# Optimization experiments

Measured on AMD Instinct MI355X. Metric: run time of the kernel, lower is better.

Reference implementation:

```python
import jax, jax.numpy as jnp
import numpy as np

EPS = 1e-5  # nn.LayerNorm default

def _ln(x, g, b):
    m = x.mean(-1, keepdims=True)
    v = ((x - m) ** 2).mean(-1, keepdims=True)
    return (x - m) / jnp.sqrt(v + EPS) * g + b


def setup_inputs() -> dict:
    key = jax.random.key(0)
    ks = jax.random.split(key, 16)
    B, T, H, W = 8, 20, 224, 224
    D, NC = 1536, 7
    s = 0.02
    f32 = jnp.float32
    return {
        'x': jax.random.normal(ks[0], (B, 3, T, H, W), f32),
        'timestamp': jax.random.uniform(ks[1], (B,), f32),
        # surrogate backbone: patchify conv (stride 16) + global avg pool -> 1536 feats
        'conv_w': jax.random.normal(ks[2], (D, 3, 16, 16), f32) * s,
        'conv_b': jnp.zeros((D,), f32),
        'w_red': jax.random.normal(ks[3], (D, D), f32) * s,
        'b_red': jnp.zeros((D,), f32),
        'w_num': jax.random.normal(ks[4], (D, 1), f32) * s,
        'b_num': jnp.zeros((D,), f32),
        'time_embed': jax.random.normal(ks[5], (1, T, D), f32) * s,
        'cls_swap': jax.random.normal(ks[6], (1, 5, 1, D), f32) * s,
        'ln_g': jnp.ones((D,), f32),
        'ln_b': jnp.zeros((D,), f32),
        'w_qkv': jax.random.normal(ks[7], (3 * D, D), f32) * s,
        'w_tproj': jax.random.normal(ks[8], (D, D), f32) * s,
        'b_tproj': jnp.zeros((D,), f32),
        'w_tfc': jax.random.normal(ks[9], (D, D), f32) * s,
        'b_tfc': jnp.zeros((D,), f32),
        'w_head': jax.random.normal(ks[10], (NC, D), f32) * s,
        'b_head': jnp.zeros((NC,), f32),
    }


def reference(x, timestamp, conv_w, conv_b, w_red, b_red, w_num, b_num,
              time_embed, cls_swap, ln_g, ln_b, w_qkv, w_tproj, b_tproj,
              w_tfc, b_tfc, w_head, b_head):
    B, C, T, H, W = x.shape
    D = w_red.shape[0]
    NH = 12
    HD = D // NH
    scale = HD ** -0.5

    # (b t) c h w  -> backbone surrogate -> (B*T, D)
    xf = jnp.transpose(x, (0, 2, 1, 3, 4)).reshape(B * T, C, H, W)
    f = jax.lax.conv_general_dilated(
        xf, conv_w, window_strides=(16, 16), padding='VALID',
        dimension_numbers=('NCHW', 'OIHW', 'NCHW'))
    f = (f + conv_b[None, :, None, None]).mean((2, 3))  # global avg pool -> (BT, D)

    xr = (f @ w_red.T + b_red).reshape(B, T, D)           # reduce_dim
    xt = xr + time_embed
    te = timestamp[:, None] @ w_num.T + b_num             # NumberToVector (B, D)
    xt = xt + te[:, None, :]

    # groups: b (n k) c -> b n k c, k=4, n=5; prepend 1 cls token per group
    g = jnp.concatenate(
        [jnp.broadcast_to(cls_swap, (B, 5, 1, D)), xt.reshape(B, 5, 4, D)], axis=2)

    for _ in range(4):  # num_interactions
        gr = g.reshape(B * 5, 5, D)
        hn = _ln(gr, ln_g, ln_b)
        qkv = (hn @ w_qkv.T).reshape(B * 5, 5, 3, NH, HD).transpose(2, 0, 3, 1, 4)
        q, k, v = qkv[0], qkv[1], qkv[2]                  # (b*n, h, t, hd)
        a = jax.nn.softmax(jnp.einsum('bhqd,bhkd->bhqk', q, k) * scale, axis=-1)
        o = jnp.einsum('bhqk,bhkd->bhqd', a, v).transpose(0, 2, 1, 3).reshape(B * 5, 5, D)
        o = o @ w_tproj.T + b_tproj                       # attn proj
        upd = (o @ w_tfc.T + b_tfc) + gr                  # temporal_fc + residual
        g = upd.reshape(B, 5, 5, D)
        # swap cls tokens between groups via roll
        g = g.at[:, :, 0, :].set(jnp.roll(g[:, :, 0, :], 1, axis=1))

    xt = g[:, :, 1:, :].reshape(B, T, D)
    out = xt[:, -1, :] + xr[:, -1, :]
    return out @ w_head.T + b_head  # (B, num_classes)
```

## Files before the change

### kernel.cpp

```cpp
#include <hip/hip_runtime.h>

typedef __attribute__((ext_vector_type(8))) short short8;
typedef __attribute__((ext_vector_type(8))) unsigned short ushort8;
typedef __attribute__((ext_vector_type(4))) float f32x4;
typedef unsigned short ushort_t;

__device__ __forceinline__ ushort_t f2bf(float f) {
    unsigned u = __builtin_bit_cast(unsigned, f);
    u += 0x7fffu + ((u >> 16) & 1u);
    return (ushort_t)(u >> 16);
}

__device__ __forceinline__ void load_lds16(const void* gp, void* lp) {
    __builtin_amdgcn_global_load_lds(
        (const __attribute__((address_space(1))) void*)gp,
        (__attribute__((address_space(3))) void*)lp, 16, 0, 0);
}

__global__ __launch_bounds__(256, 4) void pool_kernel(
    const float* __restrict__ x, ushort_t* __restrict__ AP) {
    int blk = blockIdx.x, tid = threadIdx.x;
    int bt = blk / 12, rc = blk % 12;
    int c = rc >> 2, igrp = rc & 3;
    int w = tid >> 6, lane = tid & 63;
    int i = igrp * 4 + w;
    int b = bt / 20, t = bt % 20;
    const float* base = x + (size_t)((b * 3 + c) * 20 + t) * 50176;

    f32x4 v[13];
    #pragma unroll
    for (int it = 0; it < 13; ++it) {
        int k = lane + it * 64;
        int kk = k < 784 ? k : 0;
        int ri = (kk * 9363) >> 19;
        int c4 = kk - ri * 56;
        v[it] = *(const f32x4*)(base + (16 * ri + i) * 224 + 4 * c4);
        if (k >= 784) v[it] = (f32x4){0.f, 0.f, 0.f, 0.f};
    }
    #pragma unroll
    for (int s = 1; s < 13; s <<= 1)
        #pragma unroll
        for (int j = 0; j + s < 13; j += 2 * s)
            v[j] += v[j + s];
    f32x4 acc = v[0];
    #pragma unroll
    for (int m = 4; m <= 32; m <<= 1) {
        acc[0] += __shfl_xor(acc[0], m);
        acc[1] += __shfl_xor(acc[1], m);
        acc[2] += __shfl_xor(acc[2], m);
        acc[3] += __shfl_xor(acc[3], m);
    }
    if (lane < 4) {
        ushort4 o;
        o.x = f2bf(acc[0] * (1.f / 196.f));
        o.y = f2bf(acc[1] * (1.f / 196.f));
        o.z = f2bf(acc[2] * (1.f / 196.f));
        o.w = f2bf(acc[3] * (1.f / 196.f));
        *(ushort4*)(AP + (size_t)bt * 768 + c * 256 + i * 16 + 4 * lane) = o;
    }
}

__global__ __launch_bounds__(256) void wprep_kernel(
    const float* __restrict__ w_qkv, const float* __restrict__ w_tf,
    const float* __restrict__ w_red, const float* __restrict__ conv_w,
    const float* __restrict__ w_tp, const float* __restrict__ b_tp,
    const float* __restrict__ b_tf, const float* __restrict__ conv_b,
    const float* __restrict__ b_red, const float* __restrict__ cls,
    ushort_t* __restrict__ WQ, ushort_t* __restrict__ WF,
    ushort_t* __restrict__ WR, ushort_t* __restrict__ WCVT,
    ushort_t* __restrict__ WTT, float* __restrict__ BC,
    float* __restrict__ BC2, float* __restrict__ GA) {
    __shared__ __align__(16) float smem[64 * 68];
    int blk = blockIdx.x, tid = threadIdx.x;
    if (blk < 5760) {
        long c = (long)blk * 256 + tid;
        const float* s; ushort_t* d; long i;
        if (c < 884736)       { s = w_qkv; d = WQ; i = c; }
        else if (c < 1179648) { s = w_tf;  d = WF; i = c - 884736; }
        else                  { s = w_red; d = WR; i = c - 1179648; }
        i <<= 3;
        f32x4 a = *(const f32x4*)(s + i);
        f32x4 b = *(const f32x4*)(s + i + 4);
        ushort8 o;
        o[0] = f2bf(a[0]); o[1] = f2bf(a[1]); o[2] = f2bf(a[2]); o[3] = f2bf(a[3]);
        o[4] = f2bf(b[0]); o[5] = f2bf(b[1]); o[6] = f2bf(b[2]); o[7] = f2bf(b[3]);
        *(ushort8*)(d + i) = o;
    } else if (blk < 6336) {
        int tb = blk - 5760;
        int bi = tb / 24, bj = tb % 24;
        int r0 = (tid >> 4) << 2;
        int c0 = (tid & 15) << 2;
        #pragma unroll
        for (int rr = 0; rr < 4; ++rr) {
            f32x4 v = *(const f32x4*)(w_tp + (size_t)(bi * 64 + r0 + rr) * 1536 + bj * 64 + c0);
            smem[(r0 + rr) * 68 + c0 + 0] = v[0];
            smem[(r0 + rr) * 68 + c0 + 1] = v[1];
            smem[(r0 + rr) * 68 + c0 + 2] = v[2];
            smem[(r0 + rr) * 68 + c0 + 3] = v[3];
        }
        __syncthreads();
        #pragma unroll
        for (int rr = 0; rr < 4; ++rr) {
            int jj = r0 + rr;
            ushort4 o;
            o.x = f2bf(smem[(c0 + 0) * 68 + jj]);
            o.y = f2bf(smem[(c0 + 1) * 68 + jj]);
            o.z = f2bf(smem[(c0 + 2) * 68 + jj]);
            o.w = f2bf(smem[(c0 + 3) * 68 + jj]);
            *(ushort4*)(WTT + (size_t)(bj * 64 + jj) * 1536 + bi * 64 + c0) = o;
        }
    } else if (blk < 6624) {
        int tb = blk - 6336;
        int bi = tb / 12, bj = tb % 12;
        int r0 = (tid >> 4) << 2;
        int c0 = (tid & 15) << 2;
        #pragma unroll
        for (int rr = 0; rr < 4; ++rr) {
            f32x4 v = *(const f32x4*)(conv_w + (size_t)(bi * 64 + r0 + rr) * 768 + bj * 64 + c0);
            smem[(r0 + rr) * 68 + c0 + 0] = v[0];
            smem[(r0 + rr) * 68 + c0 + 1] = v[1];
            smem[(r0 + rr) * 68 + c0 + 2] = v[2];
            smem[(r0 + rr) * 68 + c0 + 3] = v[3];
        }
        __syncthreads();
        #pragma unroll
        for (int rr = 0; rr < 4; ++rr) {
            int jj = r0 + rr;
            ushort4 o;
            o.x = f2bf(smem[(c0 + 0) * 68 + jj]);
            o.y = f2bf(smem[(c0 + 1) * 68 + jj]);
            o.z = f2bf(smem[(c0 + 2) * 68 + jj]);
            o.w = f2bf(smem[(c0 + 3) * 68 + jj]);
            *(ushort4*)(WCVT + (size_t)(bj * 64 + jj) * 1536 + bi * 64 + c0) = o;
        }
    } else if (blk < 6664) {
        int cblk = blk - 6624;
        int b = cblk / 5, n = cblk % 5;
        size_t row = (size_t)(b * 25 + n * 5) * 1536;
        #pragma unroll
        for (int j = 0; j < 6; ++j) {
            int d = tid + j * 256;
            GA[row + d] = cls[n * 1536 + d];
        }
    } else if (blk < 6760) {
        int bb = blk - 6664;
        int row = bb * 16 + (tid >> 4);
        int sub = tid & 15;
        float acc = 0.f;
        for (int j = 0; j < 96; ++j) {
            int k = sub + j * 16;
            acc += w_tf[(size_t)row * 1536 + k] * b_tp[k];
        }
        acc += __shfl_xor(acc, 1); acc += __shfl_xor(acc, 2);
        acc += __shfl_xor(acc, 4); acc += __shfl_xor(acc, 8);
        if (sub == 0) BC[row] = acc + b_tf[row];
    } else {
        int bb = blk - 6760;
        int row = bb * 16 + (tid >> 4);
        int sub = tid & 15;
        float acc = 0.f;
        for (int j = 0; j < 48; ++j) {
            int k = sub + j * 16;
            acc += w_red[(size_t)row * 1536 + k] * 0.f;
        }
        acc = 0.f;
        for (int j = 0; j < 48; ++j) {
            int n0 = sub + j * 16;
            acc += w_red[(size_t)row * 1536 + n0] * conv_b[n0];
            acc += w_red[(size_t)row * 1536 + n0 + 768] * conv_b[n0 + 768];
        }
        acc += __shfl_xor(acc, 1); acc += __shfl_xor(acc, 2);
        acc += __shfl_xor(acc, 4); acc += __shfl_xor(acc, 8);
        if (sub == 0) BC2[row] = acc + b_red[row];
    }
}

template <int MT, bool OUT_BF16, bool HAS_BIAS, bool HAS_RES, bool CLS_SWAP, bool BUILD_G>
__device__ __forceinline__ void gemm_tile(
    char* lds, int lane, int tn, int tm,
    const ushort_t* __restrict__ A, const ushort_t* __restrict__ B,
    void* __restrict__ Cv, const float* __restrict__ bias,
    const float* __restrict__ res, int M, int N, int K, int KS,
    float* __restrict__ g_out, const float* __restrict__ temb,
    const float* __restrict__ ts, const float* __restrict__ w_num,
    const float* __restrict__ b_num) {
    constexpr int BUFB = MT * 2048 + 8192;

    f32x4 acc[MT][4];
    #pragma unroll
    for (int m = 0; m < MT; ++m)
        #pragma unroll
        for (int n = 0; n < 4; ++n)
            acc[m][n] = (f32x4){0.f, 0.f, 0.f, 0.f};

    const int nK = K >> 6;
    const int rbase = lane >> 3, cc = lane & 7;

    auto stage = [&](int k0, int buf) {
        char* lA = lds + buf * BUFB;
        char* lB = lA + MT * 2048;
        #pragma unroll
        for (int j = 0; j < MT * 2; ++j) {
            int row = j * 8 + rbase;
            int cf = cc ^ (row & 7);
            int ga = tm * (MT * 16) + row; if (ga > M - 1) ga = M - 1;
            load_lds16(A + (size_t)ga * KS + (k0 + cf * 8), lA + j * 1024);
        }
        #pragma unroll
        for (int j = 0; j < 8; ++j) {
            int row = j * 8 + rbase;
            int cf = cc ^ (row & 7);
            load_lds16(B + (size_t)(tn * 64 + row) * KS + (k0 + cf * 8), lB + j * 1024);
        }
    };

    stage(0, 0);
    for (int t = 0; t < nK; ++t) {
        int cur = t & 1;
        if (t + 1 < nK) {
            stage((t + 1) << 6, cur ^ 1);
            if constexpr (MT == 2) asm volatile("s_waitcnt vmcnt(12)" ::: "memory");
            else                   asm volatile("s_waitcnt vmcnt(16)" ::: "memory");
        } else {
            asm volatile("s_waitcnt vmcnt(0)" ::: "memory");
        }
        __builtin_amdgcn_sched_barrier(0);
        const char* lA = lds + cur * BUFB;
        const char* lB = lA + MT * 2048;
        #pragma unroll
        for (int ks = 0; ks < 2; ++ks) {
            short8 av[MT], bv[4];
            const int rlo = lane & 15;
            const int chi = ks * 4 + (lane >> 4);
            #pragma unroll
            for (int m = 0; m < MT; ++m) {
                int r = m * 16 + rlo;
                av[m] = *(const short8*)(lA + r * 128 + ((chi ^ (r & 7)) << 4));
            }
            #pragma unroll
            for (int n = 0; n < 4; ++n) {
                int r = n * 16 + rlo;
                bv[n] = *(const short8*)(lB + r * 128 + ((chi ^ (r & 7)) << 4));
            }
            #pragma unroll
            for (int m = 0; m < MT; ++m)
                #pragma unroll
                for (int n = 0; n < 4; ++n)
                    acc[m][n] = __builtin_amdgcn_mfma_f32_16x16x32_bf16(
                        av[m], bv[n], acc[m][n], 0, 0, 0);
        }
    }

    const int c_l = lane & 15, r_q = (lane >> 4) * 4;
    #pragma unroll
    for (int m = 0; m < MT; ++m) {
        #pragma unroll
        for (int reg = 0; reg < 4; ++reg) {
            int r_ = tm * (MT * 16) + m * 16 + r_q + reg;
            if (r_ < M) {
                int r2 = r_;
                if (CLS_SWAP) {
                    int bb = r_ / 25, rem = r_ % 25;
                    if (rem % 5 == 0) r2 = bb * 25 + ((rem / 5 + 1) % 5) * 5;
                }
                #pragma unroll
                for (int n = 0; n < 4; ++n) {
                    int cc_ = tn * 64 + n * 16 + c_l;
                    float v = acc[m][n][reg];
                    if (HAS_BIAS) v += bias[cc_];
                    if (HAS_RES) v += res[(size_t)r_ * N + cc_];
                    if (OUT_BF16) ((ushort_t*)Cv)[(size_t)r2 * N + cc_] = f2bf(v);
                    else          ((float*)Cv)[(size_t)r2 * N + cc_] = v;
                    if (BUILD_G) {
                        int b = r_ / 20, t = r_ % 20;
                        float gval = v + temb[t * 1536 + cc_] +
                                     ts[b] * w_num[cc_] + b_num[cc_];
                        g_out[(size_t)(b * 25 + (t / 4) * 5 + (t % 4) + 1) * 1536 + cc_] = gval;
                    }
                }
            }
        }
    }
}

__global__ __launch_bounds__(64) void wcf_kernel(
    const ushort_t* __restrict__ WF, const ushort_t* __restrict__ WTT,
    const ushort_t* __restrict__ WR, const ushort_t* __restrict__ WCVT,
    ushort_t* __restrict__ WC, ushort_t* __restrict__ WRC) {
    __shared__ __align__(16) char lds[32768];
    int task = blockIdx.x, lane = threadIdx.x;
    if (task < 576)
        gemm_tile<4, true, false, false, false, false>(
            lds, lane, task % 24, task / 24, WF, WTT, WC, nullptr, nullptr,
            1536, 1536, 1536, 1536, nullptr, nullptr, nullptr, nullptr, nullptr);
    else {
        int t2 = task - 576;
        gemm_tile<4, true, false, false, false, false>(
            lds, lane, t2 % 12, t2 / 12, WR, WCVT, WRC, nullptr, nullptr,
            1536, 768, 1536, 1536, nullptr, nullptr, nullptr, nullptr, nullptr);
    }
}

__global__ __launch_bounds__(64) void xr_kernel(
    const ushort_t* __restrict__ AP, const ushort_t* __restrict__ WRC,
    float* __restrict__ XR, const float* __restrict__ BC2,
    float* __restrict__ GA, const float* __restrict__ temb,
    const float* __restrict__ ts, const float* __restrict__ w_num,
    const float* __restrict__ b_num) {
    __shared__ __align__(16) char lds[24576];
    gemm_tile<2, false, true, false, false, true>(
        lds, threadIdx.x, blockIdx.x, blockIdx.y, AP, WRC, XR, BC2, nullptr,
        160, 1536, 768, 768, GA, temb, ts, w_num, b_num);
}

__global__ __launch_bounds__(64) void qkv_kernel(
    const ushort_t* __restrict__ HN, const ushort_t* __restrict__ WQ,
    float* __restrict__ C0, float* __restrict__ C1) {
    __shared__ __align__(16) char lds[32768];
    int tn = blockIdx.x, tmh = blockIdx.y;
    int half = tmh >> 2, tm = tmh & 3;
    gemm_tile<4, false, false, false, false, false>(
        lds, threadIdx.x, tn, tm, HN + half * 768, WQ + half * 768,
        half ? C1 : C0, nullptr, nullptr, 200, 4608, 768, 1536,
        nullptr, nullptr, nullptr, nullptr, nullptr);
}

__global__ __launch_bounds__(64) void proj_kernel(
    const ushort_t* __restrict__ OBF, const ushort_t* __restrict__ WC,
    float* __restrict__ gdst, const float* __restrict__ BC,
    const float* __restrict__ gsrc) {
    __shared__ __align__(16) char lds[24576];
    gemm_tile<2, false, true, true, true, false>(
        lds, threadIdx.x, blockIdx.x, blockIdx.y, OBF, WC, gdst, BC, gsrc,
        200, 1536, 1536, 1536, nullptr, nullptr, nullptr, nullptr, nullptr);
}

__global__ __launch_bounds__(256) void ln_kernel(
    const float* __restrict__ g, const float* __restrict__ gamma,
    const float* __restrict__ beta, ushort_t* __restrict__ hn) {
    int r = blockIdx.x, tid = threadIdx.x;
    const float* x = g + (size_t)r * 1536;
    float v[6], s = 0.f, s2 = 0.f;
    #pragma unroll
    for (int j = 0; j < 6; ++j) {
        v[j] = x[tid + j * 256];
        s += v[j]; s2 += v[j] * v[j];
    }
    #pragma unroll
    for (int m = 1; m < 64; m <<= 1) { s += __shfl_xor(s, m); s2 += __shfl_xor(s2, m); }
    __shared__ float red[8];
    int wid = tid >> 6;
    if ((tid & 63) == 0) { red[wid] = s; red[4 + wid] = s2; }
    __syncthreads();
    s  = red[0] + red[1] + red[2] + red[3];
    s2 = red[4] + red[5] + red[6] + red[7];
    float mean = s * (1.0f / 1536.0f);
    float var  = s2 * (1.0f / 1536.0f) - mean * mean;
    float rstd = rsqrtf(var + 1e-5f);
    #pragma unroll
    for (int j = 0; j < 6; ++j) {
        int d = tid + j * 256;
        float y = (v[j] - mean) * rstd * gamma[d] + beta[d];
        hn[(size_t)r * 1536 + d] = f2bf(y);
    }
}

__global__ __launch_bounds__(64) void attn_kernel(
    const float* __restrict__ qA, const float* __restrict__ qB,
    ushort_t* __restrict__ o) {
    int gid = blockIdx.x;
    int h = gid % 12, gg = gid / 12;
    int l = threadIdx.x;
    size_t off = (size_t)gg * 5 * 4608 + h * 128 + 2 * l;
    const float* b0 = qA + off;
    const float* b1 = qB + off;
    float q[5][2], k[5][2], v[5][2];
    #pragma unroll
    for (int tt = 0; tt < 5; ++tt) {
        float2 q0 = *(const float2*)(b0 + tt * 4608);
        float2 q1 = *(const float2*)(b1 + tt * 4608);
        float2 k0 = *(const float2*)(b0 + tt * 4608 + 1536);
        float2 k1 = *(const float2*)(b1 + tt * 4608 + 1536);
        float2 v0 = *(const float2*)(b0 + tt * 4608 + 3072);
        float2 v1 = *(const float2*)(b1 + tt * 4608 + 3072);
        q[tt][0] = q0.x + q1.x; q[tt][1] = q0.y + q1.y;
        k[tt][0] = k0.x + k1.x; k[tt][1] = k0.y + k1.y;
        v[tt][0] = v0.x + v1.x; v[tt][1] = v0.y + v1.y;
    }
    float sc[5][5];
    #pragma unroll
    for (int i = 0; i < 5; ++i)
        #pragma unroll
        for (int j = 0; j < 5; ++j)
            sc[i][j] = q[i][0] * k[j][0] + q[i][1] * k[j][1];
    #pragma unroll
    for (int m = 1; m < 64; m <<= 1)
        #pragma unroll
        for (int i = 0; i < 5; ++i)
            #pragma unroll
            for (int j = 0; j < 5; ++j)
                sc[i][j] += __shfl_xor(sc[i][j], m);
    const float scale = 0.08838834764831845f;
    float a_[5][5];
    #pragma unroll
    for (int i = 0; i < 5; ++i) {
        float mx = -1e30f;
        #pragma unroll
        for (int j = 0; j < 5; ++j) mx = fmaxf(mx, sc[i][j]);
        float sum = 0.f;
        #pragma unroll
        for (int j = 0; j < 5; ++j) { a_[i][j] = __expf((sc[i][j] - mx) * scale); sum += a_[i][j]; }
        float inv = 1.0f / sum;
        #pragma unroll
        for (int j = 0; j < 5; ++j) a_[i][j] *= inv;
    }
    #pragma unroll
    for (int i = 0; i < 5; ++i) {
        float o0 = 0.f, o1 = 0.f;
        #pragma unroll
        for (int j = 0; j < 5; ++j) { o0 += a_[i][j] * v[j][0]; o1 += a_[i][j] * v[j][1]; }
        ushort2 w; w.x = f2bf(o0); w.y = f2bf(o1);
        *(ushort2*)(o + (size_t)(gg * 5 + i) * 1536 + h * 128 + 2 * l) = w;
    }
}

__global__ __launch_bounds__(64) void head_kernel(
    const float* __restrict__ gfin, const float* __restrict__ xr,
    const float* __restrict__ w_head, const float* __restrict__ b_head,
    float* __restrict__ out) {
    int b = blockIdx.x, l = threadIdx.x;
    const float* gv = gfin + (size_t)(b * 25 + 24) * 1536;
    const float* xv = xr + (size_t)(b * 20 + 19) * 1536;
    float acc[7] = {0, 0, 0, 0, 0, 0, 0};
    for (int d = l; d < 1536; d += 64) {
        float xval = gv[d] + xv[d];
        #pragma unroll
        for (int c = 0; c < 7; ++c) acc[c] += xval * w_head[c * 1536 + d];
    }
    #pragma unroll
    for (int c = 0; c < 7; ++c)
        #pragma unroll
        for (int m = 1; m < 64; m <<= 1) acc[c] += __shfl_xor(acc[c], m);
    if (l == 0) {
        #pragma unroll
        for (int c = 0; c < 7; ++c) out[b * 7 + c] = acc[c] + b_head[c];
    }
}

#define OFF_WQ    0u
#define OFF_WF    14155776u
#define OFF_WR    18874368u
#define OFF_WCVT  23592960u
#define OFF_WTT   25952256u
#define OFF_WC    30670848u
#define OFF_WRC   35389440u
#define OFF_BC    37748736u
#define OFF_BC2   37754880u
#define OFF_AP    37761024u
#define OFF_XR    38006784u
#define OFF_GA    38989824u
#define OFF_GB    40218624u
#define OFF_HN    41447424u
#define OFF_QKV0  42061824u
#define OFF_QKV1  45748224u
#define OFF_OBF   49434624u

extern "C" void kernel_launch(void* const* d_in, const int* in_sizes, int n_in,
                              void* d_out, int out_size, void* d_ws, size_t ws_size,
                              hipStream_t stream) {
    const float* x      = (const float*)d_in[0];
    const float* ts     = (const float*)d_in[1];
    const float* conv_w = (const float*)d_in[2];
    const float* conv_b = (const float*)d_in[3];
    const float* w_red  = (const float*)d_in[4];
    const float* b_red  = (const float*)d_in[5];
    const float* w_num  = (const float*)d_in[6];
    const float* b_num  = (const float*)d_in[7];
    const float* temb   = (const float*)d_in[8];
    const float* cls    = (const float*)d_in[9];
    const float* ln_g   = (const float*)d_in[10];
    const float* ln_b   = (const float*)d_in[11];
    const float* w_qkv  = (const float*)d_in[12];
    const float* w_tp   = (const float*)d_in[13];
    const float* b_tp   = (const float*)d_in[14];
    const float* w_tf   = (const float*)d_in[15];
    const float* b_tf   = (const float*)d_in[16];
    const float* w_head = (const float*)d_in[17];
    const float* b_head = (const float*)d_in[18];

    char* ws = (char*)d_ws;
    ushort_t* WQ   = (ushort_t*)(ws + OFF_WQ);
    ushort_t* WF   = (ushort_t*)(ws + OFF_WF);
    ushort_t* WR   = (ushort_t*)(ws + OFF_WR);
    ushort_t* WCVT = (ushort_t*)(ws + OFF_WCVT);
    ushort_t* WTT  = (ushort_t*)(ws + OFF_WTT);
    ushort_t* WC   = (ushort_t*)(ws + OFF_WC);
    ushort_t* WRC  = (ushort_t*)(ws + OFF_WRC);
    float*    BC   = (float*)(ws + OFF_BC);
    float*    BC2  = (float*)(ws + OFF_BC2);
    ushort_t* AP   = (ushort_t*)(ws + OFF_AP);
    float*    XR   = (float*)(ws + OFF_XR);
    float*    GA   = (float*)(ws + OFF_GA);
    float*    GB   = (float*)(ws + OFF_GB);
    ushort_t* HN   = (ushort_t*)(ws + OFF_HN);
    float*    QKV0 = (float*)(ws + OFF_QKV0);
    float*    QKV1 = (float*)(ws + OFF_QKV1);
    ushort_t* OBF  = (ushort_t*)(ws + OFF_OBF);

    pool_kernel<<<1920, 256, 0, stream>>>(x, AP);
    wprep_kernel<<<6856, 256, 0, stream>>>(w_qkv, w_tf, w_red, conv_w, w_tp,
                                           b_tp, b_tf, conv_b, b_red, cls,
                                           WQ, WF, WR, WCVT, WTT, BC, BC2, GA);
    wcf_kernel<<<864, 64, 0, stream>>>(WF, WTT, WR, WCVT, WC, WRC);
    xr_kernel<<<dim3(24, 5), 64, 0, stream>>>(AP, WRC, XR, BC2, GA,
                                              temb, ts, w_num, b_num);
    float* gsrc = GA;
    float* gdst = GB;
    for (int it = 0; it < 4; ++it) {
        ln_kernel<<<200, 256, 0, stream>>>(gsrc, ln_g, ln_b, HN);
        qkv_kernel<<<dim3(72, 8), 64, 0, stream>>>(HN, WQ, QKV0, QKV1);
        attn_kernel<<<480, 64, 0, stream>>>(QKV0, QKV1, OBF);
        proj_kernel<<<dim3(24, 7), 64, 0, stream>>>(OBF, WC, gdst, BC, gsrc);
        float* tmp = gsrc; gsrc = gdst; gdst = tmp;
    }
    head_kernel<<<8, 64, 0, stream>>>(gsrc, XR, w_head, b_head, (float*)d_out);
}
```

Measured before the change: 203.9 us.

## Use 128x128 four-wave double-buffered GEMM tiles for weight-fold and QKV

Adds a 256-thread GEMM tile routine computing 128x128 outputs with swizzled LDS, direct global-to-LDS loads and double buffering. The weight-folding GEMMs and the per-iteration QKV GEMM use it instead of the single-wave 64-wide tiles, aiming for more operand reuse and better latency hiding. It also removes a dead loop in the bias-fold prep. The trade-off is fewer blocks (216 and 144), which can underfill the GPU, especially for QKV with M=200, where the second 128-row tile is mostly clamped padding.

```diff
diff --git a/kernel.cpp b/kernel.cpp
--- a/kernel.cpp
+++ b/kernel.cpp
@@ -160,11 +160,6 @@
         int sub = tid & 15;
         float acc = 0.f;
         for (int j = 0; j < 48; ++j) {
-            int k = sub + j * 16;
-            acc += w_red[(size_t)row * 1536 + k] * 0.f;
-        }
-        acc = 0.f;
-        for (int j = 0; j < 48; ++j) {
             int n0 = sub + j * 16;
             acc += w_red[(size_t)row * 1536 + n0] * conv_b[n0];
             acc += w_red[(size_t)row * 1536 + n0 + 768] * conv_b[n0 + 768];
@@ -173,6 +168,127 @@
         acc += __shfl_xor(acc, 4); acc += __shfl_xor(acc, 8);
         if (sub == 0) BC2[row] = acc + b_red[row];
     }
+}
+
+template <bool OUT_BF16>
+__device__ __forceinline__ void gemm128_tile(
+    char* lds, const ushort_t* __restrict__ A, const ushort_t* __restrict__ B,
+    void* __restrict__ Cv, int M, int N, int K, int KS, int tn, int tm) {
+    const int tid = threadIdx.x;
+    const int lane = tid & 63;
+    const int w = tid >> 6;
+    const int wr = w >> 1, wc = w & 1;
+
+    f32x4 acc[4][4];
+    #pragma unroll
+    for (int m = 0; m < 4; ++m)
+        #pragma unroll
+        for (int n = 0; n < 4; ++n)
+            acc[m][n] = (f32x4){0.f, 0.f, 0.f, 0.f};
+
+    const int nK = K >> 6;
+    const int rbase = lane >> 3, cc = lane & 7;
+
+    auto stage = [&](int k0, int buf) {
+        char* lA = lds + buf * 32768;
+        char* lB = lA + 16384;
+        #pragma unroll
+        for (int j = 0; j < 4; ++j) {
+            int row = w * 32 + j * 8 + rbase;
+            int cf = cc ^ (row & 7);
+            int ga = tm * 128 + row; if (ga > M - 1) ga = M - 1;
+            load_lds16(A + (size_t)ga * KS + (k0 + cf * 8),
+                       lA + (w * 32 + j * 8) * 128);
+        }
+        #pragma unroll
+        for (int j = 0; j < 4; ++j) {
+            int row = w * 32 + j * 8 + rbase;
+            int cf = cc ^ (row & 7);
+            load_lds16(B + (size_t)(tn * 128 + row) * KS + (k0 + cf * 8),
+                       lB + (w * 32 + j * 8) * 128);
+        }
+    };
+
+    stage(0, 0);
+    asm volatile("s_waitcnt vmcnt(0)" ::: "memory");
+    __builtin_amdgcn_s_barrier();
+    __builtin_amdgcn_sched_barrier(0);
+    for (int t = 0; t < nK; ++t) {
+        int cur = t & 1;
+        if (t + 1 < nK) stage((t + 1) << 6, cur ^ 1);
+        __builtin_amdgcn_sched_barrier(0);
+        const char* lA = lds + cur * 32768;
+        const char* lB = lA + 16384;
+        #pragma unroll
+        for (int ks = 0; ks < 2; ++ks) {
+            short8 av[4], bv[4];
+            const int rlo = lane & 15;
+            const int chi = ks * 4 + (lane >> 4);
+            #pragma unroll
+            for (int m = 0; m < 4; ++m) {
+                int r = wr * 64 + m * 16 + rlo;
+                av[m] = *(const short8*)(lA + r * 128 + ((chi ^ (r & 7)) << 4));
+            }
+            #pragma unroll
+            for (int n = 0; n < 4; ++n) {
+                int r = wc * 64 + n * 16 + rlo;
+                bv[n] = *(const short8*)(lB + r * 128 + ((chi ^ (r & 7)) << 4));
+            }
+            #pragma unroll
+            for (int m = 0; m < 4; ++m)
+                #pragma unroll
+                for (int n = 0; n < 4; ++n)
+                    acc[m][n] = __builtin_amdgcn_mfma_f32_16x16x32_bf16(
+                        av[m], bv[n], acc[m][n], 0, 0, 0);
+        }
+        asm volatile("s_waitcnt vmcnt(0)" ::: "memory");
+        __builtin_amdgcn_s_barrier();
+        __builtin_amdgcn_sched_barrier(0);
+    }
+
+    const int c_l = lane & 15, r_q = (lane >> 4) * 4;
+    #pragma unroll
+    for (int m = 0; m < 4; ++m) {
+        #pragma unroll
+        for (int reg = 0; reg < 4; ++reg) {
+            int r_ = tm * 128 + wr * 64 + m * 16 + r_q + reg;
+            if (r_ < M) {
+                #pragma unroll
+                for (int n = 0; n < 4; ++n) {
+                    int cc_ = tn * 128 + wc * 64 + n * 16 + c_l;
+                    float v = acc[m][n][reg];
+                    if (OUT_BF16) ((ushort_t*)Cv)[(size_t)r_ * N + cc_] = f2bf(v);
+                    else          ((float*)Cv)[(size_t)r_ * N + cc_] = v;
+                }
+            }
+        }
+    }
+}
+
+__global__ __launch_bounds__(256) void wcf_kernel(
+    const ushort_t* __restrict__ WF, const ushort_t* __restrict__ WTT,
+    const ushort_t* __restrict__ WR, const ushort_t* __restrict__ WCVT,
+    ushort_t* __restrict__ WC, ushort_t* __restrict__ WRC) {
+    __shared__ __align__(16) char lds[65536];
+    int task = blockIdx.x;
+    if (task < 144)
+        gemm128_tile<true>(lds, WF, WTT, WC, 1536, 1536, 1536, 1536,
+                           task % 12, task / 12);
+    else {
+        int t2 = task - 144;
+        gemm128_tile<true>(lds, WR, WCVT, WRC, 1536, 768, 1536, 1536,
+                           t2 % 6, t2 / 6);
+    }
+}
+
+__global__ __launch_bounds__(256) void qkv_kernel(
+    const ushort_t* __restrict__ HN, const ushort_t* __restrict__ WQ,
+    float* __restrict__ C0, float* __restrict__ C1) {
+    __shared__ __align__(16) char lds[65536];
+    int tn = blockIdx.x, y = blockIdx.y;
+    int half = y >> 1, tm = y & 1;
+    gemm128_tile<false>(lds, HN + half * 768, WQ + half * 768,
+                        half ? C1 : C0, 200, 4608, 768, 1536, tn, tm);
 }
 
 template <int MT, bool OUT_BF16, bool HAS_BIAS, bool HAS_RES, bool CLS_SWAP, bool BUILD_G>
@@ -283,24 +399,6 @@
     }
 }
 
-__global__ __launch_bounds__(64) void wcf_kernel(
-    const ushort_t* __restrict__ WF, const ushort_t* __restrict__ WTT,
-    const ushort_t* __restrict__ WR, const ushort_t* __restrict__ WCVT,
-    ushort_t* __restrict__ WC, ushort_t* __restrict__ WRC) {
-    __shared__ __align__(16) char lds[32768];
-    int task = blockIdx.x, lane = threadIdx.x;
-    if (task < 576)
-        gemm_tile<4, true, false, false, false, false>(
-            lds, lane, task % 24, task / 24, WF, WTT, WC, nullptr, nullptr,
-            1536, 1536, 1536, 1536, nullptr, nullptr, nullptr, nullptr, nullptr);
-    else {
-        int t2 = task - 576;
-        gemm_tile<4, true, false, false, false, false>(
-            lds, lane, t2 % 12, t2 / 12, WR, WCVT, WRC, nullptr, nullptr,
-            1536, 768, 1536, 1536, nullptr, nullptr, nullptr, nullptr, nullptr);
-    }
-}
-
 __global__ __launch_bounds__(64) void xr_kernel(
     const ushort_t* __restrict__ AP, const ushort_t* __restrict__ WRC,
     float* __restrict__ XR, const float* __restrict__ BC2,
@@ -311,18 +409,6 @@
     gemm_tile<2, false, true, false, false, true>(
         lds, threadIdx.x, blockIdx.x, blockIdx.y, AP, WRC, XR, BC2, nullptr,
         160, 1536, 768, 768, GA, temb, ts, w_num, b_num);
-}
-
-__global__ __launch_bounds__(64) void qkv_kernel(
-    const ushort_t* __restrict__ HN, const ushort_t* __restrict__ WQ,
-    float* __restrict__ C0, float* __restrict__ C1) {
-    __shared__ __align__(16) char lds[32768];
-    int tn = blockIdx.x, tmh = blockIdx.y;
-    int half = tmh >> 2, tm = tmh & 3;
-    gemm_tile<4, false, false, false, false, false>(
-        lds, threadIdx.x, tn, tm, HN + half * 768, WQ + half * 768,
-        half ? C1 : C0, nullptr, nullptr, 200, 4608, 768, 1536,
-        nullptr, nullptr, nullptr, nullptr, nullptr);
 }
 
 __global__ __launch_bounds__(64) void proj_kernel(
@@ -511,14 +597,14 @@
     wprep_kernel<<<6856, 256, 0, stream>>>(w_qkv, w_tf, w_red, conv_w, w_tp,
                                            b_tp, b_tf, conv_b, b_red, cls,
                                            WQ, WF, WR, WCVT, WTT, BC, BC2, GA);
-    wcf_kernel<<<864, 64, 0, stream>>>(WF, WTT, WR, WCVT, WC, WRC);
+    wcf_kernel<<<216, 256, 0, stream>>>(WF, WTT, WR, WCVT, WC, WRC);
     xr_kernel<<<dim3(24, 5), 64, 0, stream>>>(AP, WRC, XR, BC2, GA,
                                               temb, ts, w_num, b_num);
     float* gsrc = GA;
     float* gdst = GB;
     for (int it = 0; it < 4; ++it) {
         ln_kernel<<<200, 256, 0, stream>>>(gsrc, ln_g, ln_b, HN);
-        qkv_kernel<<<dim3(72, 8), 64, 0, stream>>>(HN, WQ, QKV0, QKV1);
+        qkv_kernel<<<dim3(36, 4), 256, 0, stream>>>(HN, WQ, QKV0, QKV1);
         attn_kernel<<<480, 64, 0, stream>>>(QKV0, QKV1, OBF);
         proj_kernel<<<dim3(24, 7), 64, 0, stream>>>(OBF, WC, gdst, BC, gsrc);
         float* tmp = gsrc; gsrc = gdst; gdst = tmp;
```

Result: no change. 207.7 us (+1.9%).

## Defer fused weight-product GEMM into first QKV launch to overlap work

Applied to the files above, without the earlier changes.

The WF·WTT weight-combination GEMM moves out of the early wcf launch and into the first iteration's QKV launch, so both run as independent tiles in one grid. Only the WR·WCVT product stays before xr_kernel, which is the only one xr_kernel needs. The intent is to shorten the critical path before the xr/LN stages and let the combined-weight GEMM fill the otherwise underused grid of the first QKV GEMM. A dead loop that multiplied by zero in the bias precompute is also removed.

```diff
diff --git a/kernel.cpp b/kernel.cpp
--- a/kernel.cpp
+++ b/kernel.cpp
@@ -160,11 +160,6 @@
         int sub = tid & 15;
         float acc = 0.f;
         for (int j = 0; j < 48; ++j) {
-            int k = sub + j * 16;
-            acc += w_red[(size_t)row * 1536 + k] * 0.f;
-        }
-        acc = 0.f;
-        for (int j = 0; j < 48; ++j) {
             int n0 = sub + j * 16;
             acc += w_red[(size_t)row * 1536 + n0] * conv_b[n0];
             acc += w_red[(size_t)row * 1536 + n0 + 768] * conv_b[n0 + 768];
@@ -283,22 +278,48 @@
     }
 }
 
-__global__ __launch_bounds__(64) void wcf_kernel(
+__global__ __launch_bounds__(64) void wrc_kernel(
+    const ushort_t* __restrict__ WR, const ushort_t* __restrict__ WCVT,
+    ushort_t* __restrict__ WRC) {
+    __shared__ __align__(16) char lds[32768];
+    int task = blockIdx.x;
+    gemm_tile<4, true, false, false, false, false>(
+        lds, threadIdx.x, task % 12, task / 12, WR, WCVT, WRC, nullptr, nullptr,
+        1536, 768, 1536, 1536, nullptr, nullptr, nullptr, nullptr, nullptr);
+}
+
+__global__ __launch_bounds__(64) void qkv0wc_kernel(
+    const ushort_t* __restrict__ HN, const ushort_t* __restrict__ WQ,
+    float* __restrict__ C0, float* __restrict__ C1,
     const ushort_t* __restrict__ WF, const ushort_t* __restrict__ WTT,
-    const ushort_t* __restrict__ WR, const ushort_t* __restrict__ WCVT,
-    ushort_t* __restrict__ WC, ushort_t* __restrict__ WRC) {
+    ushort_t* __restrict__ WC) {
     __shared__ __align__(16) char lds[32768];
     int task = blockIdx.x, lane = threadIdx.x;
-    if (task < 576)
-        gemm_tile<4, true, false, false, false, false>(
-            lds, lane, task % 24, task / 24, WF, WTT, WC, nullptr, nullptr,
-            1536, 1536, 1536, 1536, nullptr, nullptr, nullptr, nullptr, nullptr);
-    else {
+    if (task < 576) {
+        int tn = task % 72, tmh = task / 72;
+        int half = tmh >> 2, tm = tmh & 3;
+        gemm_tile<4, false, false, false, false, false>(
+            lds, lane, tn, tm, HN + half * 768, WQ + half * 768,
+            half ? C1 : C0, nullptr, nullptr, 200, 4608, 768, 1536,
+            nullptr, nullptr, nullptr, nullptr, nullptr);
+    } else {
         int t2 = task - 576;
         gemm_tile<4, true, false, false, false, false>(
-            lds, lane, t2 % 12, t2 / 12, WR, WCVT, WRC, nullptr, nullptr,
-            1536, 768, 1536, 1536, nullptr, nullptr, nullptr, nullptr, nullptr);
-    }
+            lds, lane, t2 % 24, t2 / 24, WF, WTT, WC, nullptr, nullptr,
+            1536, 1536, 1536, 1536, nullptr, nullptr, nullptr, nullptr, nullptr);
+    }
+}
+
+__global__ __launch_bounds__(64) void qkv_kernel(
+    const ushort_t* __restrict__ HN, const ushort_t* __restrict__ WQ,
+    float* __restrict__ C0, float* __restrict__ C1) {
+    __shared__ __align__(16) char lds[32768];
+    int tn = blockIdx.x, tmh = blockIdx.y;
+    int half = tmh >> 2, tm = tmh & 3;
+    gemm_tile<4, false, false, false, false, false>(
+        lds, threadIdx.x, tn, tm, HN + half * 768, WQ + half * 768,
+        half ? C1 : C0, nullptr, nullptr, 200, 4608, 768, 1536,
+        nullptr, nullptr, nullptr, nullptr, nullptr);
 }
 
 __global__ __launch_bounds__(64) void xr_kernel(
@@ -311,18 +332,6 @@
     gemm_tile<2, false, true, false, false, true>(
         lds, threadIdx.x, blockIdx.x, blockIdx.y, AP, WRC, XR, BC2, nullptr,
         160, 1536, 768, 768, GA, temb, ts, w_num, b_num);
-}
-
-__global__ __launch_bounds__(64) void qkv_kernel(
-    const ushort_t* __restrict__ HN, const ushort_t* __restrict__ WQ,
-    float* __restrict__ C0, float* __restrict__ C1) {
-    __shared__ __align__(16) char lds[32768];
-    int tn = blockIdx.x, tmh = blockIdx.y;
-    int half = tmh >> 2, tm = tmh & 3;
-    gemm_tile<4, false, false, false, false, false>(
-        lds, threadIdx.x, tn, tm, HN + half * 768, WQ + half * 768,
-        half ? C1 : C0, nullptr, nullptr, 200, 4608, 768, 1536,
-        nullptr, nullptr, nullptr, nullptr, nullptr);
 }
 
 __global__ __launch_bounds__(64) void proj_kernel(
@@ -511,14 +520,18 @@
     wprep_kernel<<<6856, 256, 0, stream>>>(w_qkv, w_tf, w_red, conv_w, w_tp,
                                            b_tp, b_tf, conv_b, b_red, cls,
                                            WQ, WF, WR, WCVT, WTT, BC, BC2, GA);
-    wcf_kernel<<<864, 64, 0, stream>>>(WF, WTT, WR, WCVT, WC, WRC);
+    wrc_kernel<<<288, 64, 0, stream>>>(WR, WCVT, WRC);
     xr_kernel<<<dim3(24, 5), 64, 0, stream>>>(AP, WRC, XR, BC2, GA,
                                               temb, ts, w_num, b_num);
     float* gsrc = GA;
     float* gdst = GB;
     for (int it = 0; it < 4; ++it) {
         ln_kernel<<<200, 256, 0, stream>>>(gsrc, ln_g, ln_b, HN);
-        qkv_kernel<<<dim3(72, 8), 64, 0, stream>>>(HN, WQ, QKV0, QKV1);
+        if (it == 0)
+            qkv0wc_kernel<<<1152, 64, 0, stream>>>(HN, WQ, QKV0, QKV1,
+                                                   WF, WTT, WC);
+        else
+            qkv_kernel<<<dim3(72, 8), 64, 0, stream>>>(HN, WQ, QKV0, QKV1);
         attn_kernel<<<480, 64, 0, stream>>>(QKV0, QKV1, OBF);
         proj_kernel<<<dim3(24, 7), 64, 0, stream>>>(OBF, WC, gdst, BC, gsrc);
         float* tmp = gsrc; gsrc = gdst; gdst = tmp;
```

After: 211.7 us. +3.8%, slower.
